# Kernel optimization log

Measured on AMD Instinct MI355X. Metric: run time of the kernel, lower is better.

## Reference

```python
import jax, jax.numpy as jnp
import numpy as np


def setup_inputs() -> dict:
    key = jax.random.key(0)
    x = jax.random.uniform(key, (256, 1024), dtype=jnp.float32)  # probabilities in [0,1]
    return {"x": x, "bit_size": 256}


def reference(x, bit_size):
    # For each scalar p: exact bitstream with round(p*N) ones, randomly shuffled.
    # Vectorized: draw uniform noise per (element, bit), rank the noise within each
    # bitstream (a uniformly random permutation), and set bit=1 where rank < n_ones.
    key = jax.random.key(42)
    u = jax.random.uniform(key, x.shape + (bit_size,))          # [..., N]
    rank = jnp.argsort(jnp.argsort(u, axis=-1), axis=-1)        # random ranks 0..N-1
    n_ones = jnp.round(x * bit_size).astype(jnp.int32)[..., None]  # [..., 1]
    bits = (rank < n_ones).astype(x.dtype)                      # [..., N]
    return bits
```

## Files before the change

### kernel.cpp

```cpp
#include <hip/hip_runtime.h>

typedef unsigned int u32;
typedef unsigned long long u64;


__device__ __forceinline__ u32 rotl32(u32 x, int r) {
  return (x << r) | (x >> (32 - r));
}

__device__ __forceinline__ u32 threefry_xor(u32 i) {
  const u32 ks0 = 0u;
  const u32 ks1 = 42u;
  const u32 ks2 = 0x1BD11BF0u;
  u32 x0 = 0u + ks0;
  u32 x1 = i + ks1;
#define TFR(r) { x0 += x1; x1 = rotl32(x1, (r)); x1 ^= x0; }
  TFR(13) TFR(15) TFR(26) TFR(6)
  x0 += ks1; x1 += ks2 + 1u;
  TFR(17) TFR(29) TFR(16) TFR(24)
  x0 += ks2; x1 += ks0 + 2u;
  TFR(13) TFR(15) TFR(26) TFR(6)
  x0 += ks0; x1 += ks1 + 3u;
  TFR(17) TFR(29) TFR(16) TFR(24)
  x0 += ks1; x1 += ks2 + 4u;
  TFR(13) TFR(15) TFR(26) TFR(6)
  x0 += ks2; x1 += ks0 + 5u;
#undef TFR
  return x0 ^ x1;
}

__device__ __forceinline__ u32 rand23(u32 i) {
  return threefry_xor(i) >> 9;
}

__device__ __forceinline__ int mbcnt64(u64 m) {
  return (int)__builtin_amdgcn_mbcnt_hi((u32)(m >> 32),
              __builtin_amdgcn_mbcnt_lo((u32)m, 0u));
}

__global__ __launch_bounds__(256) void bitinput_kernel(
    const float* __restrict__ x, float* __restrict__ out, int nrows) {
  const int lane = threadIdx.x & 63;
  const int wid  = threadIdx.x >> 6;
  const int row  = (blockIdx.x << 2) + wid;
  if (row >= nrows) return;

  const float xe = x[row];
  const u32 base = ((u32)row) << 8;
  const u32 ci   = base + ((u32)lane << 2);

  u32 v0 = rand23(ci + 0u);
  u32 v1 = rand23(ci + 1u);
  u32 v2 = rand23(ci + 2u);
  u32 v3 = rand23(ci + 3u);

  const int n1 = __builtin_amdgcn_readfirstlane((int)rintf(xe * 256.0f));

  u32 T = 0u;
  int  L = 0;
  for (int bit = 22; bit >= 0; --bit) {
    const u32 mid = T | (1u << bit);
    const int cnt = __popcll(__ballot(v0 < mid)) + __popcll(__ballot(v1 < mid))
                  + __popcll(__ballot(v2 < mid)) + __popcll(__ballot(v3 < mid));
    if (cnt == n1) { T = mid; L = cnt; break; }
    if (cnt <  n1) { T = mid; L = cnt; }
  }
  const int E = n1 - L;

  const int p0 = (v0 == T), p1 = (v1 == T), p2 = (v2 == T), p3 = (v3 == T);
  const u64 m0 = __ballot(p0), m1 = __ballot(p1);
  const u64 m2 = __ballot(p2), m3 = __ballot(p3);
  const int S = mbcnt64(m0) + mbcnt64(m1) + mbcnt64(m2) + mbcnt64(m3);

  float4 o;
  o.x = (v0 < T || (p0 && (S               ) < E)) ? 1.0f : 0.0f;
  o.y = (v1 < T || (p1 && (S + p0          ) < E)) ? 1.0f : 0.0f;
  o.z = (v2 < T || (p2 && (S + p0 + p1     ) < E)) ? 1.0f : 0.0f;
  o.w = (v3 < T || (p3 && (S + p0 + p1 + p2) < E)) ? 1.0f : 0.0f;

  reinterpret_cast<float4*>(out)[(int)(base >> 2) + lane] = o;
}

extern "C" void kernel_launch(void* const* d_in, const int* in_sizes, int n_in,
                              void* d_out, int out_size, void* d_ws, size_t ws_size,
                              hipStream_t stream) {
  const float* x = (const float*)d_in[0];
  float* out = (float*)d_out;
  const int nrows = in_sizes[0];
  const int blocks = (nrows + 3) >> 2;
  hipLaunchKernelGGL(bitinput_kernel, dim3(blocks), dim3(256), 0, stream,
                     x, out, nrows);
}
```

Baseline: 349.9 us.

## Process four bitstreams per wave with unique index-tiebroken keys in radix select

Each wavefront now handles four rows instead of one, interleaving their radix-select threshold searches so the ballot/popcount chains of independent rows can overlap. The random values are packed with their in-stream index into unique 31-bit keys, which removes the separate tie-breaking pass with mbcnt but lengthens the search to 31 bits. The grid shrinks fourfold, so there are fewer waves and more registers per thread, which reduces available parallelism in exchange for ILP.

```diff
diff --git a/kernel.cpp b/kernel.cpp
--- a/kernel.cpp
+++ b/kernel.cpp
@@ -29,56 +29,61 @@
   return x0 ^ x1;
 }
 
-__device__ __forceinline__ u32 rand23(u32 i) {
-  return threefry_xor(i) >> 9;
-}
-
-__device__ __forceinline__ int mbcnt64(u64 m) {
-  return (int)__builtin_amdgcn_mbcnt_hi((u32)(m >> 32),
-              __builtin_amdgcn_mbcnt_lo((u32)m, 0u));
-}
-
 __global__ __launch_bounds__(256) void bitinput_kernel(
     const float* __restrict__ x, float* __restrict__ out, int nrows) {
-  const int lane = threadIdx.x & 63;
-  const int wid  = threadIdx.x >> 6;
-  const int row  = (blockIdx.x << 2) + wid;
-  if (row >= nrows) return;
+  const int lane  = threadIdx.x & 63;
+  const int wid   = threadIdx.x >> 6;
+  const int row0  = ((blockIdx.x << 2) + wid) << 2;
+  if (row0 >= nrows) return;
 
-  const float xe = x[row];
-  const u32 base = ((u32)row) << 8;
-  const u32 ci   = base + ((u32)lane << 2);
+  const u32 idx0 = (u32)lane << 2;
 
-  u32 v0 = rand23(ci + 0u);
-  u32 v1 = rand23(ci + 1u);
-  u32 v2 = rand23(ci + 2u);
-  u32 v3 = rand23(ci + 3u);
+  u32 K[4][4];
+#pragma unroll
+  for (int r = 0; r < 4; ++r) {
+    const u32 gbase = ((u32)(row0 + r)) << 8;
+#pragma unroll
+    for (int k = 0; k < 4; ++k) {
+      const u32 b = idx0 + (u32)k;
+      K[r][k] = ((threefry_xor(gbase + b) >> 9) << 8) | b;
+    }
+  }
 
-  const int n1 = __builtin_amdgcn_readfirstlane((int)rintf(xe * 256.0f));
+  int n1[4];
+#pragma unroll
+  for (int r = 0; r < 4; ++r)
+    n1[r] = __builtin_amdgcn_readfirstlane((int)rintf(x[row0 + r] * 256.0f));
 
-  u32 T = 0u;
-  int  L = 0;
-  for (int bit = 22; bit >= 0; --bit) {
-    const u32 mid = T | (1u << bit);
-    const int cnt = __popcll(__ballot(v0 < mid)) + __popcll(__ballot(v1 < mid))
-                  + __popcll(__ballot(v2 < mid)) + __popcll(__ballot(v3 < mid));
-    if (cnt == n1) { T = mid; L = cnt; break; }
-    if (cnt <  n1) { T = mid; L = cnt; }
+  u32 T[4]    = {0u, 0u, 0u, 0u};
+  u32 done[4] = {0u, 0u, 0u, 0u};
+#pragma unroll 1
+  for (int bit = 30; bit >= 0; --bit) {
+    const u32 b = 1u << bit;
+#pragma unroll
+    for (int r = 0; r < 4; ++r) {
+      const u32 mid = T[r] | b;
+      const int cnt = __popcll(__ballot(K[r][0] < mid))
+                    + __popcll(__ballot(K[r][1] < mid))
+                    + __popcll(__ballot(K[r][2] < mid))
+                    + __popcll(__ballot(K[r][3] < mid));
+      const u32 take = (done[r] == 0u) & (u32)(cnt <= n1[r]);
+      T[r] = take ? mid : T[r];
+      done[r] |= (u32)(cnt == n1[r]);
+    }
+    if (done[0] & done[1] & done[2] & done[3]) break;
   }
-  const int E = n1 - L;
 
-  const int p0 = (v0 == T), p1 = (v1 == T), p2 = (v2 == T), p3 = (v3 == T);
-  const u64 m0 = __ballot(p0), m1 = __ballot(p1);
-  const u64 m2 = __ballot(p2), m3 = __ballot(p3);
-  const int S = mbcnt64(m0) + mbcnt64(m1) + mbcnt64(m2) + mbcnt64(m3);
-
-  float4 o;
-  o.x = (v0 < T || (p0 && (S               ) < E)) ? 1.0f : 0.0f;
-  o.y = (v1 < T || (p1 && (S + p0          ) < E)) ? 1.0f : 0.0f;
-  o.z = (v2 < T || (p2 && (S + p0 + p1     ) < E)) ? 1.0f : 0.0f;
-  o.w = (v3 < T || (p3 && (S + p0 + p1 + p2) < E)) ? 1.0f : 0.0f;
-
-  reinterpret_cast<float4*>(out)[(int)(base >> 2) + lane] = o;
+#pragma unroll
+  for (int r = 0; r < 4; ++r) {
+    u32 Tsel = done[r] ? T[r] : (T[r] + 1u);
+    if (n1[r] == 0) Tsel = 0u;
+    float4 o;
+    o.x = (K[r][0] < Tsel) ? 1.0f : 0.0f;
+    o.y = (K[r][1] < Tsel) ? 1.0f : 0.0f;
+    o.z = (K[r][2] < Tsel) ? 1.0f : 0.0f;
+    o.w = (K[r][3] < Tsel) ? 1.0f : 0.0f;
+    reinterpret_cast<float4*>(out)[((row0 + r) << 6) + lane] = o;
+  }
 }
 
 extern "C" void kernel_launch(void* const* d_in, const int* in_sizes, int n_in,
@@ -87,7 +92,7 @@
   const float* x = (const float*)d_in[0];
   float* out = (float*)d_out;
   const int nrows = in_sizes[0];
-  const int blocks = (nrows + 3) >> 2;
+  const int blocks = (nrows + 15) >> 4;
   hipLaunchKernelGGL(bitinput_kernel, dim3(blocks), dim3(256), 0, stream,
                      x, out, nrows);
 }
```

Result: slower. 373.9 us (+6.9%).

## Pack index into random keys to make selection tie-free and simplify output

Applied to the files above, without the earlier changes.

Each random value's low 9 bits are replaced by its position index, so keys are unique and the radix-select threshold alone decides each bit, with no tie-break pass. This removes the second ballot/mbcnt stage, at the cost of searching 32 bits instead of 23. Rotations now use the alignbit builtin and wave popcounts use inline s_bcnt1 assembly. The search loop is kept rolled and stops early once the count matches.

```diff
diff --git a/kernel.cpp b/kernel.cpp
--- a/kernel.cpp
+++ b/kernel.cpp
@@ -4,9 +4,7 @@
 typedef unsigned long long u64;
 
 
-__device__ __forceinline__ u32 rotl32(u32 x, int r) {
-  return (x << r) | (x >> (32 - r));
-}
+#define ROTL(x, r) __builtin_amdgcn_alignbit((x), (x), 32u - (r))
 
 __device__ __forceinline__ u32 threefry_xor(u32 i) {
   const u32 ks0 = 0u;
@@ -14,7 +12,7 @@
   const u32 ks2 = 0x1BD11BF0u;
   u32 x0 = 0u + ks0;
   u32 x1 = i + ks1;
-#define TFR(r) { x0 += x1; x1 = rotl32(x1, (r)); x1 ^= x0; }
+#define TFR(r) { x0 += x1; x1 = ROTL(x1, r##u); x1 ^= x0; }
   TFR(13) TFR(15) TFR(26) TFR(6)
   x0 += ks1; x1 += ks2 + 1u;
   TFR(17) TFR(29) TFR(16) TFR(24)
@@ -29,13 +27,11 @@
   return x0 ^ x1;
 }
 
-__device__ __forceinline__ u32 rand23(u32 i) {
-  return threefry_xor(i) >> 9;
-}
-
-__device__ __forceinline__ int mbcnt64(u64 m) {
-  return (int)__builtin_amdgcn_mbcnt_hi((u32)(m >> 32),
-              __builtin_amdgcn_mbcnt_lo((u32)m, 0u));
+__device__ __forceinline__ u32 bcnt(int pred) {
+  u64 m = __ballot(pred);
+  u32 c;
+  asm("s_bcnt1_i32_b64 %0, %1" : "=s"(c) : "s"(m) : "scc");
+  return c;
 }
 
 __global__ __launch_bounds__(256) void bitinput_kernel(
@@ -45,40 +41,37 @@
   const int row  = (blockIdx.x << 2) + wid;
   if (row >= nrows) return;
 
-  const float xe = x[row];
-  const u32 base = ((u32)row) << 8;
-  const u32 ci   = base + ((u32)lane << 2);
+  const u32 gbase = ((u32)row) << 8;
+  const u32 ci    = gbase + ((u32)lane << 2);
 
-  u32 v0 = rand23(ci + 0u);
-  u32 v1 = rand23(ci + 1u);
-  u32 v2 = rand23(ci + 2u);
-  u32 v3 = rand23(ci + 3u);
+  const u32 b0 = (u32)(lane << 2);
+  u32 K0 = (threefry_xor(ci + 0u) & 0xFFFFFE00u) | (b0 + 0u);
+  u32 K1 = (threefry_xor(ci + 1u) & 0xFFFFFE00u) | (b0 + 1u);
+  u32 K2 = (threefry_xor(ci + 2u) & 0xFFFFFE00u) | (b0 + 2u);
+  u32 K3 = (threefry_xor(ci + 3u) & 0xFFFFFE00u) | (b0 + 3u);
 
-  const int n1 = __builtin_amdgcn_readfirstlane((int)rintf(xe * 256.0f));
+  const u32 n1 = (u32)__builtin_amdgcn_readfirstlane((int)rintf(x[row] * 256.0f));
 
-  u32 T = 0u;
-  int  L = 0;
-  for (int bit = 22; bit >= 0; --bit) {
+  u32 T = 0u, done = 0u;
+#pragma unroll 1
+  for (int bit = 31; bit >= 0; --bit) {
     const u32 mid = T | (1u << bit);
-    const int cnt = __popcll(__ballot(v0 < mid)) + __popcll(__ballot(v1 < mid))
-                  + __popcll(__ballot(v2 < mid)) + __popcll(__ballot(v3 < mid));
-    if (cnt == n1) { T = mid; L = cnt; break; }
-    if (cnt <  n1) { T = mid; L = cnt; }
+    const u32 cnt = bcnt(K0 < mid) + bcnt(K1 < mid)
+                  + bcnt(K2 < mid) + bcnt(K3 < mid);
+    const u32 ok  = (u32)((done == 0u) & (cnt <= n1));
+    T |= (1u << bit) & (0u - ok);
+    done |= (u32)(cnt == n1);
+    if (done) break;
   }
-  const int E = n1 - L;
 
-  const int p0 = (v0 == T), p1 = (v1 == T), p2 = (v2 == T), p3 = (v3 == T);
-  const u64 m0 = __ballot(p0), m1 = __ballot(p1);
-  const u64 m2 = __ballot(p2), m3 = __ballot(p3);
-  const int S = mbcnt64(m0) + mbcnt64(m1) + mbcnt64(m2) + mbcnt64(m3);
-
+  u32 Tsel = done ? T : (T + 1u);
+  if (n1 == 0u) Tsel = 0u;
   float4 o;
-  o.x = (v0 < T || (p0 && (S               ) < E)) ? 1.0f : 0.0f;
-  o.y = (v1 < T || (p1 && (S + p0          ) < E)) ? 1.0f : 0.0f;
-  o.z = (v2 < T || (p2 && (S + p0 + p1     ) < E)) ? 1.0f : 0.0f;
-  o.w = (v3 < T || (p3 && (S + p0 + p1 + p2) < E)) ? 1.0f : 0.0f;
-
-  reinterpret_cast<float4*>(out)[(int)(base >> 2) + lane] = o;
+  o.x = (K0 < Tsel) ? 1.0f : 0.0f;
+  o.y = (K1 < Tsel) ? 1.0f : 0.0f;
+  o.z = (K2 < Tsel) ? 1.0f : 0.0f;
+  o.w = (K3 < Tsel) ? 1.0f : 0.0f;
+  reinterpret_cast<float4*>(out)[(int)(gbase >> 2) + lane] = o;
 }
 
 extern "C" void kernel_launch(void* const* d_in, const int* in_sizes, int n_in,
```

After: 338.6 us. -3.2%, faster.
